# Performance work log

Measured on AMD Instinct MI355X. Metric: run time of the kernel, lower is better.

The kernel has to match this reference:

```python
import jax, jax.numpy as jnp
import numpy as np

NUM_JOINTS = 24
V = 6890
# standard SMPL kinematic tree (parent of joint i); index 0 is the root
PARENTS = [-1, 0, 0, 0, 1, 2, 3, 4, 5, 6, 7, 8, 9, 9, 9, 12, 13, 14, 16, 17, 18, 19, 20, 21]


def rodrigues(r):
    """Axis-angle [.., 3] -> rotation matrices [.., 3, 3] (batched Rodrigues)."""
    angle = jnp.sqrt(jnp.sum(r * r, axis=-1, keepdims=True) + 1e-16)
    axis = r / angle
    c = jnp.cos(angle)[..., None]
    s = jnp.sin(angle)[..., None]
    x, y, z = axis[..., 0], axis[..., 1], axis[..., 2]
    zeros = jnp.zeros_like(x)
    K = jnp.stack([zeros, -z, y, z, zeros, -x, -y, x, zeros], axis=-1).reshape(r.shape[:-1] + (3, 3))
    outer = axis[..., :, None] * axis[..., None, :]
    eye = jnp.eye(3, dtype=r.dtype)
    return c * eye + (1.0 - c) * outer + s * K


def with_zeros(Rt):
    """[B,3,4] -> [B,4,4] homogeneous transform."""
    B = Rt.shape[0]
    bottom = jnp.broadcast_to(jnp.array([0.0, 0.0, 0.0, 1.0], Rt.dtype), (B, 1, 4))
    return jnp.concatenate([Rt, bottom], axis=1)


def setup_inputs() -> dict:
    key = jax.random.key(0)
    ks = jax.random.split(key, 8)
    B = 1024
    return {
        "pose": jax.random.normal(ks[0], (B, 72), jnp.float32) * 0.3,
        "betas": jax.random.normal(ks[1], (B, 10), jnp.float32),
        "trans": jax.random.normal(ks[2], (B, 3), jnp.float32),
        "v_template": jax.random.normal(ks[3], (V, 3), jnp.float32),
        "shapedirs": jax.random.normal(ks[4], (V, 3, 10), jnp.float32) * 0.01,
        "posedirs": jax.random.normal(ks[5], (V, 3, 207), jnp.float32) * 0.01,
        "J_regressor": jax.random.uniform(ks[6], (24, V), jnp.float32) / V,
        "weights": jax.random.uniform(ks[7], (V, 24), jnp.float32),
    }


def reference(pose, betas, trans, v_template, shapedirs, posedirs, J_regressor, weights):
    B = pose.shape[0]
    dt = pose.dtype
    # pose -> per-joint rotation matrices [B,24,3,3]
    rot = rodrigues(pose.reshape(B, NUM_JOINTS, 3))
    root_rot = rot[:, 0]
    # pose blendshape features: non-root rotations minus identity, flattened [B,207]
    pose_map = (rot[:, 1:] - jnp.eye(3, dtype=dt)).reshape(B, (NUM_JOINTS - 1) * 9)
    v_shaped = v_template[None] + jnp.einsum('vcs,bs->bvc', shapedirs, betas)   # [B,V,3]
    j = jnp.einsum('jv,bvc->bjc', J_regressor, v_shaped)                        # [B,24,3]
    naked = v_shaped + jnp.einsum('vcp,bp->bvc', posedirs, pose_map)            # [B,V,3]
    v_posed = naked  # th_offsets is None
    # forward kinematics along the fixed 24-joint tree
    results = [None] * NUM_JOINTS
    results[0] = with_zeros(jnp.concatenate([root_rot, j[:, 0, :, None]], axis=2))
    for i in range(1, NUM_JOINTS):
        p = PARENTS[i]
        rel = with_zeros(jnp.concatenate([rot[:, i], (j[:, i] - j[:, p])[:, :, None]], axis=2))
        results[i] = results[p] @ rel
    G = jnp.stack(results, axis=1)  # [B,24,4,4] global transforms
    # remove rest-pose joint locations: G_rel = G - pack(G @ [j;0])
    j_h = jnp.concatenate([j, jnp.zeros((B, NUM_JOINTS, 1), dt)], axis=-1)      # [B,24,4]
    tmp = jnp.einsum('bjpq,bjq->bjp', G, j_h)                                   # [B,24,4]
    G_rel = G - jnp.concatenate([jnp.zeros(G.shape[:-1] + (3,), dt), tmp[..., None]], axis=-1)
    # linear blend skinning
    T = jnp.einsum('bjpq,vj->bpqv', G_rel, weights)                              # [B,4,4,V]
    rest_h = jnp.concatenate(
        [v_posed.transpose(0, 2, 1), jnp.ones((B, 1, v_posed.shape[1]), dt)], axis=1)  # [B,4,V]
    verts = jnp.einsum('bpqv,bqv->bvp', T, rest_h)[:, :, :3]                     # [B,V,3]
    jtr = G[:, :, :3, 3]                                                         # [B,24,3]
    # scale=1.0, normalise=False
    verts = verts + trans[:, None]
    jtr = jtr + trans[:, None]
    return verts, jtr, v_posed, naked, G
```

## Files before the change

### kernel.cpp

```cpp
#include <hip/hip_runtime.h>
#include <math.h>

#define V_NUM 6890
#define NJ 24
#define KTOT 217
#define KP 256
#define M_DIM (V_NUM * 3)
#define MPAD 20736
#define VPAD 6912

typedef __attribute__((ext_vector_type(8))) short bf16x8;
typedef __attribute__((ext_vector_type(4))) float f32x4;

__constant__ int c_parents[NJ] = {-1,0,0,0,1,2,3,4,5,6,7,8,9,9,9,12,13,14,16,17,18,19,20,21};

__device__ __forceinline__ unsigned short f2bf(float x) {
  union { float f; unsigned int u; } v; v.f = x;
  unsigned int r = v.u + 0x7fffu + ((v.u >> 16) & 1u);
  return (unsigned short)(r >> 16);
}

#define GLOBAL_AS __attribute__((address_space(1)))
#define LDS_AS __attribute__((address_space(3)))
__device__ __forceinline__ void gl_lds16(const void* g, void* l) {
  __builtin_amdgcn_global_load_lds((const GLOBAL_AS unsigned int*)g,
                                   (LDS_AS unsigned int*)l, 16, 0, 0);
}

__global__ __launch_bounds__(256) void k_regress(
    const float* __restrict__ JR, const float* __restrict__ SD,
    const float* __restrict__ VT, float* __restrict__ JS, float* __restrict__ Jt) {
  int j = blockIdx.x;
  int tid = threadIdx.x;
  float part[33];
#pragma unroll
  for (int q = 0; q < 33; q++) part[q] = 0.f;
  for (int v = tid; v < V_NUM; v += 256) {
    float jr = JR[j * V_NUM + v];
#pragma unroll
    for (int cc = 0; cc < 3; cc++) {
      part[30 + cc] += jr * VT[v * 3 + cc];
#pragma unroll
      for (int ss = 0; ss < 10; ss++)
        part[cc * 10 + ss] += jr * SD[(v * 3 + cc) * 10 + ss];
    }
  }
  __shared__ float sm[33][4];
  int lane = tid & 63, wid = tid >> 6;
#pragma unroll
  for (int q = 0; q < 33; q++) {
    float x = part[q];
    for (int off = 32; off > 0; off >>= 1) x += __shfl_down(x, off);
    if (lane == 0) sm[q][wid] = x;
  }
  __syncthreads();
  if (tid < 33) {
    float s = sm[tid][0] + sm[tid][1] + sm[tid][2] + sm[tid][3];
    if (tid < 30) JS[j * 30 + tid] = s;
    else Jt[j * 3 + (tid - 30)] = s;
  }
}

__global__ __launch_bounds__(256) void k_conv(
    const float* __restrict__ SD, const float* __restrict__ PD,
    const float* __restrict__ W,
    unsigned short* __restrict__ Abf, unsigned short* __restrict__ Wbf) {
  int bid = blockIdx.x;
  int tid = threadIdx.x;
  if (bid < MPAD) {
    int m = bid, k = tid;
    float v = 0.f;
    if (m < M_DIM && k < KTOT)
      v = (k < 10) ? SD[(size_t)m * 10 + k] : PD[(size_t)m * 207 + (k - 10)];
    Abf[(size_t)m * KP + k] = f2bf(v);
  } else {
    int idx = (bid - MPAD) * 256 + tid;
    if (idx < VPAD * 32) {
      int v = idx >> 5, k = idx & 31;
      Wbf[idx] = (v < V_NUM && k < NJ) ? f2bf(W[(size_t)v * NJ + k]) : (unsigned short)0;
    }
  }
}

__global__ __launch_bounds__(64) void k_batch(
    const float* __restrict__ pose, const float* __restrict__ betas,
    const float* __restrict__ trans, const float* __restrict__ JS,
    const float* __restrict__ Jt, unsigned short* __restrict__ Kcb,
    unsigned short* __restrict__ GrelP, float* __restrict__ outG,
    float* __restrict__ outJtr, int B) {
  int b = blockIdx.x;
  int lane = threadIdx.x;
  __shared__ float rotS[NJ][9];
  __shared__ float jS[NJ * 3];
  __shared__ float Gs[NJ][12];
  __shared__ float GrS[NJ][12];

  if (lane < NJ) {
    float rx = pose[b * 72 + lane * 3 + 0];
    float ry = pose[b * 72 + lane * 3 + 1];
    float rz = pose[b * 72 + lane * 3 + 2];
    float a2 = rx * rx + ry * ry + rz * rz + 1e-16f;
    float ang = sqrtf(a2);
    float inv = 1.f / ang;
    float ux = rx * inv, uy = ry * inv, uz = rz * inv;
    float c = cosf(ang), s = sinf(ang), ic = 1.f - c;
    float R[9];
    R[0] = c + ic * ux * ux;      R[1] = ic * ux * uy - s * uz; R[2] = ic * ux * uz + s * uy;
    R[3] = ic * uy * ux + s * uz; R[4] = c + ic * uy * uy;      R[5] = ic * uy * uz - s * ux;
    R[6] = ic * uz * ux - s * uy; R[7] = ic * uz * uy + s * ux; R[8] = c + ic * uz * uz;
#pragma unroll
    for (int k = 0; k < 9; k++) rotS[lane][k] = R[k];
    if (lane > 0) {
#pragma unroll
      for (int k = 0; k < 9; k++) {
        float iden = (k == 0 || k == 4 || k == 8) ? 1.f : 0.f;
        Kcb[(size_t)b * KP + 10 + (lane - 1) * 9 + k] = f2bf(R[k] - iden);
      }
    }
  }
  if (lane < 10) Kcb[(size_t)b * KP + lane] = f2bf(betas[b * 10 + lane]);
  if (lane < KP - KTOT) Kcb[(size_t)b * KP + KTOT + lane] = 0;

  __syncthreads();
  for (int idx = lane; idx < 72; idx += 64) {
    float s = Jt[idx];
#pragma unroll
    for (int ss = 0; ss < 10; ss++) s += JS[idx * 10 + ss] * betas[b * 10 + ss];
    jS[idx] = s;
  }
  __syncthreads();

  if (lane == 0) {
#pragma unroll
    for (int p = 0; p < 3; p++) {
      Gs[0][p * 4 + 0] = rotS[0][p * 3 + 0];
      Gs[0][p * 4 + 1] = rotS[0][p * 3 + 1];
      Gs[0][p * 4 + 2] = rotS[0][p * 3 + 2];
      Gs[0][p * 4 + 3] = jS[p];
    }
    for (int i = 1; i < NJ; i++) {
      int par = c_parents[i];
      float t0 = jS[i * 3 + 0] - jS[par * 3 + 0];
      float t1 = jS[i * 3 + 1] - jS[par * 3 + 1];
      float t2 = jS[i * 3 + 2] - jS[par * 3 + 2];
#pragma unroll
      for (int p = 0; p < 3; p++) {
        float rp0 = Gs[par][p * 4 + 0], rp1 = Gs[par][p * 4 + 1], rp2 = Gs[par][p * 4 + 2];
#pragma unroll
        for (int q = 0; q < 3; q++) {
          Gs[i][p * 4 + q] = rp0 * rotS[i][0 * 3 + q] + rp1 * rotS[i][1 * 3 + q] + rp2 * rotS[i][2 * 3 + q];
        }
        Gs[i][p * 4 + 3] = rp0 * t0 + rp1 * t1 + rp2 * t2 + Gs[par][p * 4 + 3];
      }
    }
    for (int i = 0; i < NJ; i++) {
      float jx = jS[i * 3 + 0], jy = jS[i * 3 + 1], jz = jS[i * 3 + 2];
#pragma unroll
      for (int p = 0; p < 3; p++) {
        float g0 = Gs[i][p * 4 + 0], g1 = Gs[i][p * 4 + 1], g2 = Gs[i][p * 4 + 2];
        GrS[i][p * 4 + 0] = g0;
        GrS[i][p * 4 + 1] = g1;
        GrS[i][p * 4 + 2] = g2;
        GrS[i][p * 4 + 3] = Gs[i][p * 4 + 3] - (g0 * jx + g1 * jy + g2 * jz);
      }
    }
  }
  __syncthreads();

  for (int idx = lane; idx < NJ * 16; idx += 64) {
    int jj = idx >> 4, rc = idx & 15, p = rc >> 2, q = rc & 3;
    float val = (p < 3) ? Gs[jj][p * 4 + q] : ((q == 3) ? 1.f : 0.f);
    outG[(size_t)b * NJ * 16 + idx] = val;
  }
  for (int idx = lane; idx < NJ * 3; idx += 64) {
    int jj = idx / 3, p = idx % 3;
    outJtr[(size_t)b * NJ * 3 + idx] = Gs[jj][p * 4 + 3] + trans[b * 3 + p];
  }
  for (int idx = lane; idx < 16 * 40; idx += 64) {
    int c = idx / 40, j = idx % 40;
    GrelP[(size_t)b * 640 + idx] = (c < 12 && j < NJ) ? f2bf(GrS[j][c]) : (unsigned short)0;
  }
}

__global__ __launch_bounds__(256) void k_pose_mfma(
    const unsigned short* __restrict__ Kcb, const unsigned short* __restrict__ Abf,
    const float* __restrict__ VT, float* __restrict__ outVP, int B) {
  __shared__ char ldsraw[65536];
  float* stage = (float*)ldsraw;
  float* vtS   = (float*)(ldsraw + 17408);

  const int tid = threadIdx.x;
  const int lane = tid & 63;
  const int w = tid >> 6;
  const int wr = w >> 1, wc = w & 1;
  const int b0 = blockIdx.y * 128;
  const int m0 = blockIdx.x * 128;

  f32x4 acc[4][4];
#pragma unroll
  for (int i = 0; i < 4; i++)
#pragma unroll
    for (int j = 0; j < 4; j++) acc[i][j] = (f32x4){0.f, 0.f, 0.f, 0.f};

  int Lrow[4], Lkb[4];
#pragma unroll
  for (int i = 0; i < 4; i++) {
    int L = w * 4096 + i * 1024 + lane * 16;
    int row = L >> 7;
    int kb = (L & 127) ^ ((row & 7) << 4);
    Lrow[i] = row;
    Lkb[i] = kb >> 1;
  }

#define STAGE(kt, c)                                                              \
  {                                                                               \
    char* bufA = ldsraw + (c) * 32768;                                            \
    char* bufB = bufA + 16384;                                                    \
    _Pragma("unroll")                                                             \
    for (int i = 0; i < 4; i++) {                                                 \
      const unsigned short* gA = Kcb + (size_t)(b0 + Lrow[i]) * KP + (kt) * 64 + Lkb[i]; \
      gl_lds16(gA, bufA + w * 4096 + i * 1024);                                   \
      const unsigned short* gB = Abf + (size_t)(m0 + Lrow[i]) * KP + (kt) * 64 + Lkb[i]; \
      gl_lds16(gB, bufB + w * 4096 + i * 1024);                                   \
    }                                                                             \
  }

  STAGE(0, 0);
  __syncthreads();

#pragma unroll
  for (int kt = 0; kt < 4; ++kt) {
    int cur = kt & 1;
    if (kt < 3) STAGE(kt + 1, cur ^ 1);
    const char* At = ldsraw + cur * 32768;
    const char* Bt = At + 16384;
#pragma unroll
    for (int h = 0; h < 2; ++h) {
      bf16x8 fm[4], fb[4];
#pragma unroll
      for (int fi = 0; fi < 4; fi++) {
        int row = wr * 64 + fi * 16 + (lane & 15);
        int byte = (row << 7) + ((h * 64 + ((lane >> 4) << 4)) ^ ((row & 7) << 4));
        fm[fi] = *(const bf16x8*)(Bt + byte);
      }
#pragma unroll
      for (int fj = 0; fj < 4; fj++) {
        int row = wc * 64 + fj * 16 + (lane & 15);
        int byte = (row << 7) + ((h * 64 + ((lane >> 4) << 4)) ^ ((row & 7) << 4));
        fb[fj] = *(const bf16x8*)(At + byte);
      }
#pragma unroll
      for (int fi = 0; fi < 4; fi++)
#pragma unroll
        for (int fj = 0; fj < 4; fj++)
          acc[fi][fj] = __builtin_amdgcn_mfma_f32_16x16x32_bf16(fm[fi], fb[fj], acc[fi][fj], 0, 0, 0);
    }
    __syncthreads();
  }
#undef STAGE

  if (tid < 128) vtS[tid] = (m0 + tid < M_DIM) ? VT[m0 + tid] : 0.f;
#pragma unroll
  for (int pp = 0; pp < 4; pp++) {
    __syncthreads();
    {
      int rowIdx = wc * 16 + (lane & 15);
#pragma unroll
      for (int fi = 0; fi < 4; fi++) {
        int ml = wr * 64 + fi * 16 + ((lane >> 4) << 2);
        *(f32x4*)&stage[rowIdx * 132 + ml] = acc[fi][pp];
      }
    }
    __syncthreads();
    int row = tid >> 3;
    int brow = ((row >> 4) * 64) + pp * 16 + (row & 15);
    size_t gb = (size_t)(b0 + brow) * M_DIM;
#pragma unroll
    for (int i = 0; i < 4; i++) {
      int col4 = (tid & 7) + 8 * i;
      int mg = m0 + col4 * 4;
      f32x4 v = *(f32x4*)&stage[row * 132 + col4 * 4];
      f32x4 vt = *(f32x4*)&vtS[col4 * 4];
      v = v + vt;
      if (mg + 3 < M_DIM) {
        *(f32x4*)(outVP + gb + mg) = v;
      } else {
#pragma unroll
        for (int r = 0; r < 4; r++)
          if (mg + r < M_DIM) outVP[gb + mg + r] = v[r];
      }
    }
  }
}

__global__ __launch_bounds__(256) void k_skin6(
    const float* __restrict__ VP, const unsigned short* __restrict__ Wbf,
    const unsigned short* __restrict__ GrelP, const float* __restrict__ trans,
    float* __restrict__ outNK, float* __restrict__ outVerts, int B) {
  __shared__ float Tl[4][64 * 13];
  const int tid = threadIdx.x;
  const int lane = tid & 63;
  const int w = tid >> 6;
  const int vl16 = lane & 15;
  const int p = lane >> 4;
  const int kb = p * 8;
  const int vbase = blockIdx.x * 256 + w * 64;
  const int b0 = blockIdx.y * 8;
  const int vg = vbase + lane;
  const bool vok = vg < V_NUM;

  bf16x8 wf[4];
#pragma unroll
  for (int sub = 0; sub < 4; sub++)
    wf[sub] = *(const bf16x8*)(Wbf + (size_t)(vbase + sub * 16 + vl16) * 32 + kb);

  bf16x8 af[8];
#pragma unroll
  for (int bi = 0; bi < 8; bi++)
    af[bi] = *(const bf16x8*)(GrelP + (size_t)(b0 + bi) * 640 + vl16 * 40 + kb);

  float* myT = Tl[w];

  float xc0 = 0.f, xc1 = 0.f, xc2 = 0.f;
  if (vok) {
    const float* xp = VP + (size_t)b0 * M_DIM + (size_t)vg * 3;
    xc0 = xp[0]; xc1 = xp[1]; xc2 = xp[2];
  }

#pragma unroll
  for (int bi = 0; bi < 8; bi++) {
    int b = b0 + bi;
    f32x4 acc[4];
#pragma unroll
    for (int sub = 0; sub < 4; sub++) {
      f32x4 z = (f32x4){0.f, 0.f, 0.f, 0.f};
      acc[sub] = __builtin_amdgcn_mfma_f32_16x16x32_bf16(af[bi], wf[sub], z, 0, 0, 0);
    }
    if (p < 3) {
#pragma unroll
      for (int sub = 0; sub < 4; sub++) {
        int vi = sub * 16 + vl16;
#pragma unroll
        for (int r = 0; r < 4; r++)
          myT[vi * 13 + p * 4 + r] = acc[sub][r];
      }
    }
    float xn0 = 0.f, xn1 = 0.f, xn2 = 0.f;
    if (bi < 7 && vok) {
      const float* xp = VP + (size_t)(b + 1) * M_DIM + (size_t)vg * 3;
      xn0 = xp[0]; xn1 = xp[1]; xn2 = xp[2];
    }
    if (vok) {
      size_t base = (size_t)b * M_DIM + (size_t)vg * 3;
      float* onk = outNK + base;
      onk[0] = xc0; onk[1] = xc1; onk[2] = xc2;
      float t[12];
#pragma unroll
      for (int c = 0; c < 12; c++) t[c] = myT[lane * 13 + c];
      float* op = outVerts + base;
      op[0] = t[0] * xc0 + t[1] * xc1 + t[2] * xc2 + t[3] + trans[b * 3 + 0];
      op[1] = t[4] * xc0 + t[5] * xc1 + t[6] * xc2 + t[7] + trans[b * 3 + 1];
      op[2] = t[8] * xc0 + t[9] * xc1 + t[10] * xc2 + t[11] + trans[b * 3 + 2];
    }
    xc0 = xn0; xc1 = xn1; xc2 = xn2;
  }
}

extern "C" void kernel_launch(void* const* d_in, const int* in_sizes, int n_in,
                              void* d_out, int out_size, void* d_ws, size_t ws_size,
                              hipStream_t stream) {
  const float* pose  = (const float*)d_in[0];
  const float* betas = (const float*)d_in[1];
  const float* trans = (const float*)d_in[2];
  const float* vt    = (const float*)d_in[3];
  const float* sd    = (const float*)d_in[4];
  const float* pd    = (const float*)d_in[5];
  const float* jreg  = (const float*)d_in[6];
  const float* wgt   = (const float*)d_in[7];
  int B = in_sizes[0] / 72;

  float* out = (float*)d_out;
  size_t nvb = (size_t)B * M_DIM;
  float* o_verts = out;
  float* o_jtr   = o_verts + nvb;
  float* o_vp    = o_jtr + (size_t)B * NJ * 3;
  float* o_nk    = o_vp + nvb;
  float* o_G     = o_nk + nvb;

  char* wsb = (char*)d_ws;
  float* JS = (float*)wsb;
  float* Jt = JS + 720;
  size_t off = (720 + 72) * 4;
  unsigned short* Kcb   = (unsigned short*)(wsb + off);
  unsigned short* Abf   = (unsigned short*)(wsb + off + (size_t)B * KP * 2);
  unsigned short* GrelP = Abf + (size_t)MPAD * KP;
  unsigned short* Wbf   = GrelP + (size_t)B * 640;

  k_regress<<<24, 256, 0, stream>>>(jreg, sd, vt, JS, Jt);
  k_conv<<<MPAD + (VPAD * 32 + 255) / 256, 256, 0, stream>>>(sd, pd, wgt, Abf, Wbf);
  k_batch<<<B, 64, 0, stream>>>(pose, betas, trans, JS, Jt, Kcb, GrelP, o_G, o_jtr, B);
  dim3 gC(MPAD / 128, B / 128);
  k_pose_mfma<<<gC, 256, 0, stream>>>(Kcb, Abf, vt, o_vp, B);
  dim3 gD(VPAD / 256, B / 8);
  k_skin6<<<gD, 256, 0, stream>>>(o_vp, Wbf, GrelP, trans, o_nk, o_verts, B);
}
```

Measured before the change: 151.4 us.

## Parallelize joint regression, per-wave epilogue staging, smaller skin batch tile

Joint regression now runs as a 24x33 grid with one output per block instead of 24 blocks each computing 33 partial sums, so many more CUs take part. The pose GEMM epilogue stages accumulators through a per-wave swizzled LDS slab and loads the template offsets into registers. This removes the block-wide barriers and the shared template buffer. The skinning kernel processes 4 batch elements per block instead of 8, which doubles the grid but reloads the weight fragments more often.

After: 147.5 us. 2.6% less time.

```diff
diff --git a/kernel.cpp b/kernel.cpp
--- a/kernel.cpp
+++ b/kernel.cpp
@@ -27,37 +27,30 @@
                                    (LDS_AS unsigned int*)l, 16, 0, 0);
 }
 
-__global__ __launch_bounds__(256) void k_regress(
+__global__ __launch_bounds__(256) void k_regress2(
     const float* __restrict__ JR, const float* __restrict__ SD,
     const float* __restrict__ VT, float* __restrict__ JS, float* __restrict__ Jt) {
   int j = blockIdx.x;
+  int q = blockIdx.y;
   int tid = threadIdx.x;
-  float part[33];
-#pragma unroll
-  for (int q = 0; q < 33; q++) part[q] = 0.f;
-  for (int v = tid; v < V_NUM; v += 256) {
-    float jr = JR[j * V_NUM + v];
-#pragma unroll
-    for (int cc = 0; cc < 3; cc++) {
-      part[30 + cc] += jr * VT[v * 3 + cc];
-#pragma unroll
-      for (int ss = 0; ss < 10; ss++)
-        part[cc * 10 + ss] += jr * SD[(v * 3 + cc) * 10 + ss];
-    }
-  }
-  __shared__ float sm[33][4];
-  int lane = tid & 63, wid = tid >> 6;
-#pragma unroll
-  for (int q = 0; q < 33; q++) {
-    float x = part[q];
-    for (int off = 32; off > 0; off >>= 1) x += __shfl_down(x, off);
-    if (lane == 0) sm[q][wid] = x;
-  }
+  float part = 0.f;
+  const float* jr = JR + (size_t)j * V_NUM;
+  if (q < 30) {
+    for (int v = tid; v < V_NUM; v += 256)
+      part += jr[v] * SD[(size_t)v * 30 + q];
+  } else {
+    int cc = q - 30;
+    for (int v = tid; v < V_NUM; v += 256)
+      part += jr[v] * VT[(size_t)v * 3 + cc];
+  }
+  for (int off = 32; off > 0; off >>= 1) part += __shfl_down(part, off);
+  __shared__ float sm[4];
+  if ((tid & 63) == 0) sm[tid >> 6] = part;
   __syncthreads();
-  if (tid < 33) {
-    float s = sm[tid][0] + sm[tid][1] + sm[tid][2] + sm[tid][3];
-    if (tid < 30) JS[j * 30 + tid] = s;
-    else Jt[j * 3 + (tid - 30)] = s;
+  if (tid == 0) {
+    float s = sm[0] + sm[1] + sm[2] + sm[3];
+    if (q < 30) JS[j * 30 + q] = s;
+    else Jt[j * 3 + (q - 30)] = s;
   }
 }
 
@@ -186,8 +179,6 @@
     const unsigned short* __restrict__ Kcb, const unsigned short* __restrict__ Abf,
     const float* __restrict__ VT, float* __restrict__ outVP, int B) {
   __shared__ char ldsraw[65536];
-  float* stage = (float*)ldsraw;
-  float* vtS   = (float*)(ldsraw + 17408);
 
   const int tid = threadIdx.x;
   const int lane = tid & 63;
@@ -195,6 +186,20 @@
   const int wr = w >> 1, wc = w & 1;
   const int b0 = blockIdx.y * 128;
   const int m0 = blockIdx.x * 128;
+
+  f32x4 vt4[4];
+  {
+    int mbase = m0 + wr * 64 + ((lane >> 4) << 4);
+#pragma unroll
+    for (int i = 0; i < 4; i++) {
+      int mm = mbase + i * 4;
+      if (mm + 3 < M_DIM) vt4[i] = *(const f32x4*)(VT + mm);
+      else {
+#pragma unroll
+        for (int r = 0; r < 4; r++) vt4[i][r] = (mm + r < M_DIM) ? VT[mm + r] : 0.f;
+      }
+    }
+  }
 
   f32x4 acc[4][4];
 #pragma unroll
@@ -259,29 +264,25 @@
   }
 #undef STAGE
 
-  if (tid < 128) vtS[tid] = (m0 + tid < M_DIM) ? VT[m0 + tid] : 0.f;
-#pragma unroll
-  for (int pp = 0; pp < 4; pp++) {
-    __syncthreads();
-    {
-      int rowIdx = wc * 16 + (lane & 15);
-#pragma unroll
-      for (int fi = 0; fi < 4; fi++) {
-        int ml = wr * 64 + fi * 16 + ((lane >> 4) << 2);
-        *(f32x4*)&stage[rowIdx * 132 + ml] = acc[fi][pp];
-      }
-    }
-    __syncthreads();
-    int row = tid >> 3;
-    int brow = ((row >> 4) * 64) + pp * 16 + (row & 15);
-    size_t gb = (size_t)(b0 + brow) * M_DIM;
+  char* wslab = ldsraw + w * 4352;
+  const int a = lane & 15, c = lane >> 4;
+  const int xr = (lane & 3) << 4;
+#pragma unroll
+  for (int fj = 0; fj < 4; fj++) {
+#pragma unroll
+    for (int fi = 0; fi < 4; fi++) {
+      int off = a * 272 + (((fi << 6) + (c << 4)) ^ xr);
+      *(f32x4*)(wslab + off) = acc[fi][fj];
+    }
+    int brow = b0 + wc * 64 + fj * 16 + a;
+    size_t gb = (size_t)brow * M_DIM;
+    int mg0 = m0 + wr * 64 + (c << 4);
 #pragma unroll
     for (int i = 0; i < 4; i++) {
-      int col4 = (tid & 7) + 8 * i;
-      int mg = m0 + col4 * 4;
-      f32x4 v = *(f32x4*)&stage[row * 132 + col4 * 4];
-      f32x4 vt = *(f32x4*)&vtS[col4 * 4];
-      v = v + vt;
+      int off = a * 272 + (((c << 6) + (i << 4)) ^ xr);
+      f32x4 v = *(f32x4*)(wslab + off);
+      v = v + vt4[i];
+      int mg = mg0 + i * 4;
       if (mg + 3 < M_DIM) {
         *(f32x4*)(outVP + gb + mg) = v;
       } else {
@@ -293,7 +294,7 @@
   }
 }
 
-__global__ __launch_bounds__(256) void k_skin6(
+__global__ __launch_bounds__(256) void k_skin7(
     const float* __restrict__ VP, const unsigned short* __restrict__ Wbf,
     const unsigned short* __restrict__ GrelP, const float* __restrict__ trans,
     float* __restrict__ outNK, float* __restrict__ outVerts, int B) {
@@ -305,7 +306,7 @@
   const int p = lane >> 4;
   const int kb = p * 8;
   const int vbase = blockIdx.x * 256 + w * 64;
-  const int b0 = blockIdx.y * 8;
+  const int b0 = blockIdx.y * 4;
   const int vg = vbase + lane;
   const bool vok = vg < V_NUM;
 
@@ -314,9 +315,9 @@
   for (int sub = 0; sub < 4; sub++)
     wf[sub] = *(const bf16x8*)(Wbf + (size_t)(vbase + sub * 16 + vl16) * 32 + kb);
 
-  bf16x8 af[8];
-#pragma unroll
-  for (int bi = 0; bi < 8; bi++)
+  bf16x8 af[4];
+#pragma unroll
+  for (int bi = 0; bi < 4; bi++)
     af[bi] = *(const bf16x8*)(GrelP + (size_t)(b0 + bi) * 640 + vl16 * 40 + kb);
 
   float* myT = Tl[w];
@@ -328,7 +329,7 @@
   }
 
 #pragma unroll
-  for (int bi = 0; bi < 8; bi++) {
+  for (int bi = 0; bi < 4; bi++) {
     int b = b0 + bi;
     f32x4 acc[4];
 #pragma unroll
@@ -346,7 +347,7 @@
       }
     }
     float xn0 = 0.f, xn1 = 0.f, xn2 = 0.f;
-    if (bi < 7 && vok) {
+    if (bi < 3 && vok) {
       const float* xp = VP + (size_t)(b + 1) * M_DIM + (size_t)vg * 3;
       xn0 = xp[0]; xn1 = xp[1]; xn2 = xp[2];
     }
@@ -396,11 +397,12 @@
   unsigned short* GrelP = Abf + (size_t)MPAD * KP;
   unsigned short* Wbf   = GrelP + (size_t)B * 640;
 
-  k_regress<<<24, 256, 0, stream>>>(jreg, sd, vt, JS, Jt);
+  dim3 gR(24, 33);
+  k_regress2<<<gR, 256, 0, stream>>>(jreg, sd, vt, JS, Jt);
   k_conv<<<MPAD + (VPAD * 32 + 255) / 256, 256, 0, stream>>>(sd, pd, wgt, Abf, Wbf);
   k_batch<<<B, 64, 0, stream>>>(pose, betas, trans, JS, Jt, Kcb, GrelP, o_G, o_jtr, B);
   dim3 gC(MPAD / 128, B / 128);
   k_pose_mfma<<<gC, 256, 0, stream>>>(Kcb, Abf, vt, o_vp, B);
-  dim3 gD(VPAD / 256, B / 8);
-  k_skin6<<<gD, 256, 0, stream>>>(o_vp, Wbf, GrelP, trans, o_nk, o_verts, B);
-}
+  dim3 gD(VPAD / 256, B / 4);
+  k_skin7<<<gD, 256, 0, stream>>>(o_vp, Wbf, GrelP, trans, o_nk, o_verts, B);
+}
```
